# Kernel optimization log

Measured on AMD Instinct MI355X. Metric: run time of the kernel, lower is better.

Reference implementation:

```python
import jax, jax.numpy as jnp
import numpy as np

N = 100000
E = 1600000
IN_C = 128
HEADS = 4
HEAD_D = 32  # out_channels(128) // heads(4)


def setup_inputs() -> dict:
    key = jax.random.key(0)
    k1, k2, k3, k4, k5, k6 = jax.random.split(key, 6)
    x = jax.random.normal(k1, (N, IN_C), dtype=jnp.float32)
    edge_index = jax.random.randint(k2, (2, E), 0, N, dtype=jnp.int64)
    edge_weight = jax.random.uniform(k3, (E,), dtype=jnp.float32)
    # params: linear weight stored as [in, H*D] so forward is x @ W (torch does x @ weight.T)
    W = jax.random.normal(k4, (IN_C, HEADS * HEAD_D), dtype=jnp.float32) * (1.0 / np.sqrt(IN_C))
    att_src = jax.random.normal(k5, (HEADS, HEAD_D), dtype=jnp.float32) * 0.1
    att_dst = jax.random.normal(k6, (HEADS, HEAD_D), dtype=jnp.float32) * 0.1
    return {"x": x, "W": W, "att_src": att_src, "att_dst": att_dst,
            "edge_weight": edge_weight, "edge_index": edge_index, "num_nodes": N}


def reference(x, W, att_src, att_dst, edge_weight, edge_index, num_nodes):
    H, D = att_src.shape
    xw = (x @ W).reshape(-1, H, D)                       # [N, H, D]
    row, col = edge_index[0], edge_index[1]
    a_src = jnp.einsum('nhd,hd->nh', xw, att_src)        # [N, H]
    a_dst = jnp.einsum('nhd,hd->nh', xw, att_dst)        # [N, H]
    alpha = jax.nn.leaky_relu(a_src[row] + a_dst[col], negative_slope=0.2)  # [E, H]
    # segment softmax over edges grouped by row (destination of aggregation)
    amax = jax.ops.segment_max(alpha, row, num_segments=num_nodes)          # [N, H]
    amax = jnp.where(jnp.isfinite(amax), amax, 0.0)      # empty segments -> 0 (matches torch init)
    alpha = jnp.exp(alpha - amax[row])
    asum = jax.ops.segment_sum(alpha, row, num_segments=num_nodes)          # [N, H]
    alpha = alpha / (asum[row] + 1e-16)
    msg = xw[col] * alpha[..., None]                     # [E, H, D]
    out = jax.ops.segment_sum(msg, row, num_segments=num_nodes)             # [N, H, D]
    return out.reshape(num_nodes, H * D)
```

## Files before the change

### kernel.cpp

```cpp
#include <hip/hip_runtime.h>
#include <math.h>


typedef _Float16 half4 __attribute__((ext_vector_type(4)));
typedef _Float16 half8 __attribute__((ext_vector_type(8)));
typedef float    f32x4 __attribute__((ext_vector_type(4)));

#define PCHUNK   4096
#define NB_SHIFT 8
#define BCAP     4864

__device__ __forceinline__ float lrelu_exp(float v) {
    return __expf(fmaxf(v, 0.2f * v));
}

__global__ __launch_bounds__(256) void k_gemm(const float* __restrict__ x,
                                              const float* __restrict__ W,
                                              const float* __restrict__ att_src,
                                              const float* __restrict__ att_dst,
                                              _Float16* __restrict__ xwh,
                                              float* __restrict__ a_src,
                                              float* __restrict__ a_dst, int N) {
    __shared__ float Ws[32][128];
    __shared__ float xT[32][68];
    int t = threadIdx.x;
    int tx = t & 31;
    int ty = t >> 5;
    int row0 = blockIdx.x * 64;

    float acc[8][4];
    #pragma unroll
    for (int r = 0; r < 8; ++r)
        #pragma unroll
        for (int j = 0; j < 4; ++j) acc[r][j] = 0.f;

    for (int kc = 0; kc < 128; kc += 32) {
        __syncthreads();
        #pragma unroll
        for (int i = 0; i < 4; ++i) {
            int fi = i * 256 + t;
            int kl = fi >> 5, c4 = (fi & 31) << 2;
            *(float4*)&Ws[kl][c4] = *(const float4*)&W[(size_t)(kc + kl) * 128 + c4];
        }
        #pragma unroll
        for (int i = 0; i < 2; ++i) {
            int fi = i * 256 + t;
            int r = fi >> 3, kq = (fi & 7) << 2;
            int grow = row0 + r; if (grow >= N) grow = N - 1;
            float4 v = *(const float4*)&x[(size_t)grow * 128 + kc + kq];
            xT[kq + 0][r] = v.x;
            xT[kq + 1][r] = v.y;
            xT[kq + 2][r] = v.z;
            xT[kq + 3][r] = v.w;
        }
        __syncthreads();
        #pragma unroll 8
        for (int k = 0; k < 32; ++k) {
            float4 wv = *(const float4*)&Ws[k][tx << 2];
            float4 xa = *(const float4*)&xT[k][ty << 3];
            float4 xb = *(const float4*)&xT[k][(ty << 3) + 4];
            float xr[8] = {xa.x, xa.y, xa.z, xa.w, xb.x, xb.y, xb.z, xb.w};
            #pragma unroll
            for (int r = 0; r < 8; ++r) {
                acc[r][0] = fmaf(xr[r], wv.x, acc[r][0]);
                acc[r][1] = fmaf(xr[r], wv.y, acc[r][1]);
                acc[r][2] = fmaf(xr[r], wv.z, acc[r][2]);
                acc[r][3] = fmaf(xr[r], wv.w, acc[r][3]);
            }
        }
    }

    int h  = tx >> 3;
    int dq = (tx & 7) << 2;
    float4 as = *(const float4*)&att_src[h * 32 + dq];
    float4 ad = *(const float4*)&att_dst[h * 32 + dq];
    #pragma unroll
    for (int r = 0; r < 8; ++r) {
        int row = row0 + (ty << 3) + r;
        bool ok = row < N;
        if (ok) {
            half4 hv;
            hv.x = (_Float16)acc[r][0];
            hv.y = (_Float16)acc[r][1];
            hv.z = (_Float16)acc[r][2];
            hv.w = (_Float16)acc[r][3];
            *(half4*)&xwh[(size_t)row * 128 + (tx << 2)] = hv;
        }
        float ps = acc[r][0] * as.x + acc[r][1] * as.y + acc[r][2] * as.z + acc[r][3] * as.w;
        float pd = acc[r][0] * ad.x + acc[r][1] * ad.y + acc[r][2] * ad.z + acc[r][3] * ad.w;
        ps += __shfl_xor(ps, 1); pd += __shfl_xor(pd, 1);
        ps += __shfl_xor(ps, 2); pd += __shfl_xor(pd, 2);
        ps += __shfl_xor(ps, 4); pd += __shfl_xor(pd, 4);
        if (ok && (tx & 7) == 0) {
            a_src[(size_t)row * 4 + h] = ps;
            a_dst[(size_t)row * 4 + h] = pd;
        }
    }
}

__global__ __launch_bounds__(256) void k_part(const int* __restrict__ eidx,
                                              int* __restrict__ bctr,
                                              unsigned long long* __restrict__ rec,
                                              int E) {
    __shared__ unsigned long long buf[PCHUNK];
    __shared__ unsigned long long sbuf[PCHUNK];
    __shared__ int hist[512], excl[512], gbase[512], cur[512];
    __shared__ int wtot[4];
    int t = threadIdx.x;
    int lane = t & 63, wv = t >> 6;
    int e0 = blockIdx.x * PCHUNK;
    int nE = E - e0; if (nE > PCHUNK) nE = PCHUNK;
    hist[t] = 0; hist[t + 256] = 0;
    __syncthreads();
    for (int i = t; i < nE; i += 256) {
        int row = __builtin_nontemporal_load(&eidx[e0 + i]);
        int col = __builtin_nontemporal_load(&eidx[E + e0 + i]);
        buf[i] = ((unsigned long long)(unsigned)col << 32) | (unsigned)row;
        atomicAdd(&hist[row >> NB_SHIFT], 1);
    }
    __syncthreads();
    int h0 = hist[2 * t], h1 = hist[2 * t + 1];
    int s = h0 + h1, sc = s;
    #pragma unroll
    for (int off = 1; off < 64; off <<= 1) {
        int v = __shfl_up(sc, off);
        if (lane >= off) sc += v;
    }
    if (lane == 63) wtot[wv] = sc;
    __syncthreads();
    if (t == 0) {
        int run = 0;
        #pragma unroll
        for (int i = 0; i < 4; ++i) { int tmp = wtot[i]; wtot[i] = run; run += tmp; }
    }
    __syncthreads();
    int incl = sc + wtot[wv];
    excl[2 * t]     = incl - s;
    excl[2 * t + 1] = incl - h1;
    cur[2 * t]      = incl - s;
    cur[2 * t + 1]  = incl - h1;
    gbase[2 * t]     = h0 ? atomicAdd(&bctr[2 * t], h0) : 0;
    gbase[2 * t + 1] = h1 ? atomicAdd(&bctr[2 * t + 1], h1) : 0;
    __syncthreads();
    for (int i = t; i < nE; i += 256) {
        unsigned long long r = buf[i];
        int row = (int)(unsigned)r;
        int dst = atomicAdd(&cur[row >> NB_SHIFT], 1);
        sbuf[dst] = r;
    }
    __syncthreads();
    for (int j = t; j < nE; j += 256) {
        unsigned long long r = sbuf[j];
        int row = (int)(unsigned)r;
        int b = row >> NB_SHIFT;
        int off = gbase[b] + (j - excl[b]);
        if (off < BCAP)
            __builtin_nontemporal_store(r, &rec[(size_t)b * BCAP + off]);
    }
}

__global__ __launch_bounds__(256) void k_csr(const unsigned long long* __restrict__ rec,
                                             const int* __restrict__ bctr,
                                             int2* __restrict__ rseg,
                                             int* __restrict__ csr_col, int N) {
    __shared__ int cnt[256], cur[256];
    __shared__ int wtot[4];
    int b = blockIdx.x;
    int rs = b << NB_SHIFT;
    int t = threadIdx.x;
    int lane = t & 63, wv = t >> 6;
    cnt[t] = 0;
    __syncthreads();
    int m = bctr[b]; if (m > BCAP) m = BCAP;
    const unsigned long long* rr = &rec[(size_t)b * BCAP];
    for (int i = t; i < m; i += 256) {
        int row = (int)(unsigned)rr[i];
        atomicAdd(&cnt[row & 255], 1);
    }
    __syncthreads();
    int c = cnt[t], sc = c;
    #pragma unroll
    for (int off = 1; off < 64; off <<= 1) {
        int v = __shfl_up(sc, off);
        if (lane >= off) sc += v;
    }
    if (lane == 63) wtot[wv] = sc;
    __syncthreads();
    if (t == 0) {
        int run = 0;
        #pragma unroll
        for (int i = 0; i < 4; ++i) { int tmp = wtot[i]; wtot[i] = run; run += tmp; }
    }
    __syncthreads();
    int ex = sc + wtot[wv] - c;
    cur[t] = ex;
    int n = rs + t;
    if (n < N) {
        int2 sg;
        sg.x = b * BCAP + ex;
        sg.y = b * BCAP + ex + c;
        rseg[n] = sg;
    }
    __syncthreads();
    for (int i = t; i < m; i += 256) {
        unsigned long long r = rr[i];
        int row = (int)(unsigned)r;
        int col = (int)(r >> 32);
        int slot = atomicAdd(&cur[row & 255], 1);
        csr_col[b * BCAP + slot] = col;
    }
}

__global__ __launch_bounds__(256) void k_agg(const int2* __restrict__ rseg,
                                             const int* __restrict__ csr_col,
                                             const float* __restrict__ a_src,
                                             const float* __restrict__ a_dst,
                                             const _Float16* __restrict__ xwh,
                                             float* __restrict__ out, int N) {
    int lane = threadIdx.x & 63;
    int n = blockIdx.x * 4 + (threadIdx.x >> 6);
    if (n >= N) return;
    int2 seg = rseg[n];
    int beg = seg.x, end = seg.y;
    int q = lane >> 4;
    int l = lane & 15;
    int h = l >> 2;
    float s_n = a_src[(size_t)n * 4 + h];
    float acc[8] = {0, 0, 0, 0, 0, 0, 0, 0};
    float ws = 0.f;

    for (int w0 = beg; w0 < end; w0 += 64) {
        int rem = end - w0; if (rem > 64) rem = 64;
        int cc = (lane < rem) ? __builtin_nontemporal_load(&csr_col[w0 + lane]) : 0;
        int j = 0;
        for (; j + 16 <= rem; j += 16) {
            int c[4]; float ad[4]; half8 xv[4];
            #pragma unroll
            for (int u = 0; u < 4; ++u) c[u] = __shfl(cc, j + u * 4 + q);
            #pragma unroll
            for (int u = 0; u < 4; ++u) {
                ad[u] = a_dst[(size_t)c[u] * 4 + h];
                xv[u] = *(const half8*)&xwh[(size_t)c[u] * 128 + (l << 3)];
            }
            #pragma unroll
            for (int u = 0; u < 4; ++u) {
                float w = lrelu_exp(s_n + ad[u]);
                ws += w;
                #pragma unroll
                for (int k = 0; k < 8; ++k)
                    acc[k] += w * (float)xv[u][k];
            }
        }
        if (j < rem) {
            int c[4]; float m[4]; float ad[4]; half8 xv[4];
            #pragma unroll
            for (int u = 0; u < 4; ++u) {
                int r = j + u * 4 + q;
                c[u] = __shfl(cc, r);
                m[u] = (r < rem) ? 1.f : 0.f;
            }
            #pragma unroll
            for (int u = 0; u < 4; ++u) {
                ad[u] = a_dst[(size_t)c[u] * 4 + h];
                xv[u] = *(const half8*)&xwh[(size_t)c[u] * 128 + (l << 3)];
            }
            #pragma unroll
            for (int u = 0; u < 4; ++u) {
                float w = m[u] * lrelu_exp(s_n + ad[u]);
                ws += w;
                #pragma unroll
                for (int k = 0; k < 8; ++k)
                    acc[k] += w * (float)xv[u][k];
            }
        }
    }

    #pragma unroll
    for (int k = 0; k < 8; ++k) {
        acc[k] += __shfl_xor(acc[k], 16);
        acc[k] += __shfl_xor(acc[k], 32);
    }
    ws += __shfl_xor(ws, 16);
    ws += __shfl_xor(ws, 32);
    if (q == 0) {
        float inv = 1.0f / (ws + 1e-16f);
        f32x4 o0 = {acc[0] * inv, acc[1] * inv, acc[2] * inv, acc[3] * inv};
        f32x4 o1 = {acc[4] * inv, acc[5] * inv, acc[6] * inv, acc[7] * inv};
        __builtin_nontemporal_store(o0, (f32x4*)&out[(size_t)n * 128 + (l << 3)]);
        __builtin_nontemporal_store(o1, (f32x4*)&out[(size_t)n * 128 + (l << 3) + 4]);
    }
}

extern "C" void kernel_launch(void* const* d_in, const int* in_sizes, int n_in,
                              void* d_out, int out_size, void* d_ws, size_t ws_size,
                              hipStream_t stream) {
    const float* x       = (const float*)d_in[0];
    const float* W       = (const float*)d_in[1];
    const float* att_src = (const float*)d_in[2];
    const float* att_dst = (const float*)d_in[3];
    const int* eidx      = (const int*)d_in[5];
    int N = in_sizes[0] / 128;
    int E = in_sizes[4];
    float* out = (float*)d_out;

    char* p = (char*)d_ws;
    auto alloc = [&](size_t bytes) {
        char* r = p;
        p += (bytes + 255) & ~(size_t)255;
        return r;
    };
    int nbuckets = (N + 255) >> NB_SHIFT;
    _Float16* xwh  = (_Float16*)alloc((size_t)N * 128 * 2);
    float* a_src   = (float*)alloc((size_t)N * 4 * 4);
    float* a_dst   = (float*)alloc((size_t)N * 4 * 4);
    int*   bctr    = (int*)  alloc(512 * 4);
    unsigned long long* rec = (unsigned long long*)alloc((size_t)nbuckets * BCAP * 8);
    int2*  rseg    = (int2*) alloc((size_t)N * 8);
    int*   csr_col = (int*)  alloc((size_t)nbuckets * BCAP * 4);

    (void)hipMemsetAsync(bctr, 0, 512 * 4, stream);
    k_gemm<<<(N + 63) / 64, 256, 0, stream>>>(x, W, att_src, att_dst, xwh, a_src, a_dst, N);
    k_part<<<(E + PCHUNK - 1) / PCHUNK, 256, 0, stream>>>(eidx, bctr, rec, E);
    k_csr<<<nbuckets, 256, 0, stream>>>(rec, bctr, rseg, csr_col, N);
    k_agg<<<(N + 3) / 4, 256, 0, stream>>>(rseg, csr_col, a_src, a_dst, xwh, out, N);
}
```

Before: 271.1 us.

## Use MFMA fp16 GEMM for projection and process four nodes per wave in aggregation

The FP32 SIMT projection GEMM is replaced with an MFMA 16x16x32 fp16 kernel that converts x to half in swizzled LDS and reads a pre-transposed fp16 copy of W, prepared by a new small kernel. The aggregation kernel now gives each wave four consecutive destination nodes. When their combined edge lists fit in 128 entries it loads the column indices once and shares them by shuffle, and it sums four edges' contributions per step. This is meant to cut GEMM ALU time and per-node launch and index-load overhead, but rounding x and W to fp16 costs input precision.

```diff
diff --git a/kernel.cpp b/kernel.cpp
--- a/kernel.cpp
+++ b/kernel.cpp
@@ -14,86 +14,110 @@
     return __expf(fmaxf(v, 0.2f * v));
 }
 
+__global__ __launch_bounds__(128) void k_prep(const float* __restrict__ W,
+                                              _Float16* __restrict__ WTh) {
+    int n = blockIdx.x;
+    int k = threadIdx.x;
+    WTh[n * 128 + k] = (_Float16)W[(size_t)k * 128 + n];
+}
+
+__device__ __forceinline__ _Float16* lds_ptr(_Float16* base, int r, int kf16) {
+    int g = (kf16 >> 3) ^ (r & 7);
+    return base + r * 128 + g * 8 + (kf16 & 7);
+}
+
 __global__ __launch_bounds__(256) void k_gemm(const float* __restrict__ x,
-                                              const float* __restrict__ W,
+                                              const _Float16* __restrict__ WTh,
                                               const float* __restrict__ att_src,
                                               const float* __restrict__ att_dst,
                                               _Float16* __restrict__ xwh,
                                               float* __restrict__ a_src,
                                               float* __restrict__ a_dst, int N) {
-    __shared__ float Ws[32][128];
-    __shared__ float xT[32][68];
+    __shared__ _Float16 Xs[128 * 128];
+    __shared__ _Float16 Ws[128 * 128];
     int t = threadIdx.x;
-    int tx = t & 31;
-    int ty = t >> 5;
-    int row0 = blockIdx.x * 64;
-
-    float acc[8][4];
-    #pragma unroll
-    for (int r = 0; r < 8; ++r)
-        #pragma unroll
-        for (int j = 0; j < 4; ++j) acc[r][j] = 0.f;
-
-    for (int kc = 0; kc < 128; kc += 32) {
-        __syncthreads();
-        #pragma unroll
-        for (int i = 0; i < 4; ++i) {
-            int fi = i * 256 + t;
-            int kl = fi >> 5, c4 = (fi & 31) << 2;
-            *(float4*)&Ws[kl][c4] = *(const float4*)&W[(size_t)(kc + kl) * 128 + c4];
+    int lane = t & 63, wv = t >> 6;
+    int lm = lane & 15, lg = lane >> 4;
+    int row0 = blockIdx.x * 128;
+
+    #pragma unroll
+    for (int i = 0; i < 8; ++i) {
+        int f = (i * 256 + t) * 8;
+        int nr = f >> 7, kc = f & 127;
+        *(half8*)lds_ptr(Ws, nr, kc) = *(const half8*)&WTh[f];
+    }
+    #pragma unroll
+    for (int i = 0; i < 8; ++i) {
+        int f = (i * 256 + t) * 8;
+        int r = f >> 7, kc = f & 127;
+        int gr = row0 + r; if (gr >= N) gr = N - 1;
+        float4 v0 = *(const float4*)&x[(size_t)gr * 128 + kc];
+        float4 v1 = *(const float4*)&x[(size_t)gr * 128 + kc + 4];
+        half8 hv;
+        hv[0] = (_Float16)v0.x; hv[1] = (_Float16)v0.y;
+        hv[2] = (_Float16)v0.z; hv[3] = (_Float16)v0.w;
+        hv[4] = (_Float16)v1.x; hv[5] = (_Float16)v1.y;
+        hv[6] = (_Float16)v1.z; hv[7] = (_Float16)v1.w;
+        *(half8*)lds_ptr(Xs, r, kc) = hv;
+    }
+    __syncthreads();
+
+    f32x4 acc[2][8];
+    #pragma unroll
+    for (int m = 0; m < 2; ++m)
+        #pragma unroll
+        for (int nn = 0; nn < 8; ++nn) acc[m][nn] = (f32x4){0.f, 0.f, 0.f, 0.f};
+
+    #pragma unroll
+    for (int kk = 0; kk < 4; ++kk) {
+        int kb = kk * 32 + lg * 8;
+        half8 a0 = *(const half8*)lds_ptr(Xs, wv * 32 + lm, kb);
+        half8 a1 = *(const half8*)lds_ptr(Xs, wv * 32 + 16 + lm, kb);
+        half8 b[8];
+        #pragma unroll
+        for (int nn = 0; nn < 8; ++nn)
+            b[nn] = *(const half8*)lds_ptr(Ws, nn * 16 + lm, kb);
+        #pragma unroll
+        for (int nn = 0; nn < 8; ++nn) {
+            acc[0][nn] = __builtin_amdgcn_mfma_f32_16x16x32_f16(a0, b[nn], acc[0][nn], 0, 0, 0);
+            acc[1][nn] = __builtin_amdgcn_mfma_f32_16x16x32_f16(a1, b[nn], acc[1][nn], 0, 0, 0);
         }
-        #pragma unroll
-        for (int i = 0; i < 2; ++i) {
-            int fi = i * 256 + t;
-            int r = fi >> 3, kq = (fi & 7) << 2;
-            int grow = row0 + r; if (grow >= N) grow = N - 1;
-            float4 v = *(const float4*)&x[(size_t)grow * 128 + kc + kq];
-            xT[kq + 0][r] = v.x;
-            xT[kq + 1][r] = v.y;
-            xT[kq + 2][r] = v.z;
-            xT[kq + 3][r] = v.w;
-        }
-        __syncthreads();
-        #pragma unroll 8
-        for (int k = 0; k < 32; ++k) {
-            float4 wv = *(const float4*)&Ws[k][tx << 2];
-            float4 xa = *(const float4*)&xT[k][ty << 3];
-            float4 xb = *(const float4*)&xT[k][(ty << 3) + 4];
-            float xr[8] = {xa.x, xa.y, xa.z, xa.w, xb.x, xb.y, xb.z, xb.w};
+    }
+
+    float asv[8], adv[8];
+    #pragma unroll
+    for (int nn = 0; nn < 8; ++nn) {
+        asv[nn] = att_src[nn * 16 + lm];
+        adv[nn] = att_dst[nn * 16 + lm];
+    }
+    #pragma unroll
+    for (int m = 0; m < 2; ++m) {
+        #pragma unroll
+        for (int reg = 0; reg < 4; ++reg) {
+            int row = row0 + wv * 32 + m * 16 + lg * 4 + reg;
+            bool ok = row < N;
+            if (ok) {
+                #pragma unroll
+                for (int nn = 0; nn < 8; ++nn)
+                    xwh[(size_t)row * 128 + nn * 16 + lm] = (_Float16)acc[m][nn][reg];
+            }
+            float ps[4], pd[4];
             #pragma unroll
-            for (int r = 0; r < 8; ++r) {
-                acc[r][0] = fmaf(xr[r], wv.x, acc[r][0]);
-                acc[r][1] = fmaf(xr[r], wv.y, acc[r][1]);
-                acc[r][2] = fmaf(xr[r], wv.z, acc[r][2]);
-                acc[r][3] = fmaf(xr[r], wv.w, acc[r][3]);
-            }
-        }
-    }
-
-    int h  = tx >> 3;
-    int dq = (tx & 7) << 2;
-    float4 as = *(const float4*)&att_src[h * 32 + dq];
-    float4 ad = *(const float4*)&att_dst[h * 32 + dq];
-    #pragma unroll
-    for (int r = 0; r < 8; ++r) {
-        int row = row0 + (ty << 3) + r;
-        bool ok = row < N;
-        if (ok) {
-            half4 hv;
-            hv.x = (_Float16)acc[r][0];
-            hv.y = (_Float16)acc[r][1];
-            hv.z = (_Float16)acc[r][2];
-            hv.w = (_Float16)acc[r][3];
-            *(half4*)&xwh[(size_t)row * 128 + (tx << 2)] = hv;
-        }
-        float ps = acc[r][0] * as.x + acc[r][1] * as.y + acc[r][2] * as.z + acc[r][3] * as.w;
-        float pd = acc[r][0] * ad.x + acc[r][1] * ad.y + acc[r][2] * ad.z + acc[r][3] * ad.w;
-        ps += __shfl_xor(ps, 1); pd += __shfl_xor(pd, 1);
-        ps += __shfl_xor(ps, 2); pd += __shfl_xor(pd, 2);
-        ps += __shfl_xor(ps, 4); pd += __shfl_xor(pd, 4);
-        if (ok && (tx & 7) == 0) {
-            a_src[(size_t)row * 4 + h] = ps;
-            a_dst[(size_t)row * 4 + h] = pd;
+            for (int hh = 0; hh < 4; ++hh) {
+                ps[hh] = acc[m][2 * hh][reg] * asv[2 * hh] + acc[m][2 * hh + 1][reg] * asv[2 * hh + 1];
+                pd[hh] = acc[m][2 * hh][reg] * adv[2 * hh] + acc[m][2 * hh + 1][reg] * adv[2 * hh + 1];
+                #pragma unroll
+                for (int off = 1; off < 16; off <<= 1) {
+                    ps[hh] += __shfl_xor(ps[hh], off);
+                    pd[hh] += __shfl_xor(pd[hh], off);
+                }
+            }
+            if (ok && lm == 0) {
+                f32x4 vs = {ps[0], ps[1], ps[2], ps[3]};
+                f32x4 vd = {pd[0], pd[1], pd[2], pd[3]};
+                *(f32x4*)&a_src[(size_t)row * 4] = vs;
+                *(f32x4*)&a_dst[(size_t)row * 4] = vd;
+            }
         }
     }
 }
@@ -211,6 +235,32 @@
     }
 }
 
+#define EDGE4(C0, C1, C2, C3, M0, M1, M2, M3)                              \
+    {                                                                      \
+        float ad0 = a_dst[(size_t)(C0) * 4 + h];                           \
+        float ad1 = a_dst[(size_t)(C1) * 4 + h];                           \
+        float ad2 = a_dst[(size_t)(C2) * 4 + h];                           \
+        float ad3 = a_dst[(size_t)(C3) * 4 + h];                           \
+        half8 x0 = *(const half8*)&xwh[(size_t)(C0) * 128 + (l << 3)];     \
+        half8 x1 = *(const half8*)&xwh[(size_t)(C1) * 128 + (l << 3)];     \
+        half8 x2 = *(const half8*)&xwh[(size_t)(C2) * 128 + (l << 3)];     \
+        half8 x3 = *(const half8*)&xwh[(size_t)(C3) * 128 + (l << 3)];     \
+        float w0 = (M0) * lrelu_exp(s + ad0);                              \
+        float w1 = (M1) * lrelu_exp(s + ad1);                              \
+        float w2 = (M2) * lrelu_exp(s + ad2);                              \
+        float w3 = (M3) * lrelu_exp(s + ad3);                              \
+        ws += w0 + w1 + w2 + w3;                                           \
+        _Pragma("unroll")                                                  \
+        for (int kk = 0; kk < 8; ++kk)                                     \
+            acc[kk] += w0 * (float)x0[kk] + w1 * (float)x1[kk]             \
+                     + w2 * (float)x2[kk] + w3 * (float)x3[kk];            \
+    }
+
+#define FETCH2(IDX) ({ int _i = (IDX);                                     \
+                       int _c0 = __shfl(cc0, _i);                          \
+                       int _c1 = __shfl(cc1, _i - 64);                     \
+                       _i < 64 ? _c0 : _c1; })
+
 __global__ __launch_bounds__(256) void k_agg(const int2* __restrict__ rseg,
                                              const int* __restrict__ csr_col,
                                              const float* __restrict__ a_src,
@@ -218,76 +268,131 @@
                                              const _Float16* __restrict__ xwh,
                                              float* __restrict__ out, int N) {
     int lane = threadIdx.x & 63;
-    int n = blockIdx.x * 4 + (threadIdx.x >> 6);
-    if (n >= N) return;
-    int2 seg = rseg[n];
-    int beg = seg.x, end = seg.y;
+    int wv = threadIdx.x >> 6;
+    int n0 = (blockIdx.x * 4 + wv) * 4;
+    if (n0 >= N) return;
+    int nv = N - n0; if (nv > 4) nv = 4;
     int q = lane >> 4;
     int l = lane & 15;
     int h = l >> 2;
-    float s_n = a_src[(size_t)n * 4 + h];
-    float acc[8] = {0, 0, 0, 0, 0, 0, 0, 0};
-    float ws = 0.f;
-
-    for (int w0 = beg; w0 < end; w0 += 64) {
-        int rem = end - w0; if (rem > 64) rem = 64;
-        int cc = (lane < rem) ? __builtin_nontemporal_load(&csr_col[w0 + lane]) : 0;
-        int j = 0;
-        for (; j + 16 <= rem; j += 16) {
-            int c[4]; float ad[4]; half8 xv[4];
+
+    int begs[4], ends[4];
+    if (nv == 4) {
+        int4 sa = *(const int4*)&rseg[n0];
+        int4 sb = *(const int4*)&rseg[n0 + 2];
+        begs[0] = sa.x; ends[0] = sa.y; begs[1] = sa.z; ends[1] = sa.w;
+        begs[2] = sb.x; ends[2] = sb.y; begs[3] = sb.z; ends[3] = sb.w;
+    } else {
+        int2 s0 = rseg[n0];
+        begs[0] = s0.x; ends[0] = s0.y;
+        #pragma unroll
+        for (int j = 1; j < 4; ++j) {
+            if (j < nv) { int2 sj = rseg[n0 + j]; begs[j] = sj.x; ends[j] = sj.y; }
+            else        { begs[j] = ends[j - 1];  ends[j] = ends[j - 1]; }
+        }
+    }
+    float sn[4];
+    #pragma unroll
+    for (int j = 0; j < 4; ++j)
+        sn[j] = (j < nv) ? a_src[(size_t)(n0 + j) * 4 + h] : 0.f;
+
+    int base = begs[0];
+    int L = ends[3] - base;
+
+    if (L <= 128) {
+        int cc0 = (lane < L)      ? __builtin_nontemporal_load(&csr_col[base + lane])      : 0;
+        int cc1 = (lane + 64 < L) ? __builtin_nontemporal_load(&csr_col[base + 64 + lane]) : 0;
+        #pragma unroll
+        for (int j = 0; j < 4; ++j) {
+            float acc[8] = {0, 0, 0, 0, 0, 0, 0, 0};
+            float ws = 0.f;
+            float s = sn[j];
+            int deg = ends[j] - begs[j];
+            int o = begs[j] - base;
+            int i = 0;
+            for (; i + 16 <= deg; i += 16) {
+                int i0 = o + i + q;
+                int c0 = FETCH2(i0);
+                int c1 = FETCH2(i0 + 4);
+                int c2 = FETCH2(i0 + 8);
+                int c3 = FETCH2(i0 + 12);
+                EDGE4(c0, c1, c2, c3, 1.f, 1.f, 1.f, 1.f);
+            }
+            if (i < deg) {
+                int r0 = i + q, r1 = i + 4 + q, r2 = i + 8 + q, r3 = i + 12 + q;
+                float m0 = r0 < deg ? 1.f : 0.f;
+                float m1 = r1 < deg ? 1.f : 0.f;
+                float m2 = r2 < deg ? 1.f : 0.f;
+                float m3 = r3 < deg ? 1.f : 0.f;
+                int c0 = FETCH2(r0 < deg ? o + r0 : o);
+                int c1 = FETCH2(r1 < deg ? o + r1 : o);
+                int c2 = FETCH2(r2 < deg ? o + r2 : o);
+                int c3 = FETCH2(r3 < deg ? o + r3 : o);
+                EDGE4(c0, c1, c2, c3, m0, m1, m2, m3);
+            }
             #pragma unroll
-            for (int u = 0; u < 4; ++u) c[u] = __shfl(cc, j + u * 4 + q);
+            for (int kk = 0; kk < 8; ++kk) {
+                acc[kk] += __shfl_xor(acc[kk], 16);
+                acc[kk] += __shfl_xor(acc[kk], 32);
+            }
+            ws += __shfl_xor(ws, 16);
+            ws += __shfl_xor(ws, 32);
+            if (q == 0 && j < nv) {
+                int n = n0 + j;
+                float inv = 1.0f / (ws + 1e-16f);
+                f32x4 o0 = {acc[0] * inv, acc[1] * inv, acc[2] * inv, acc[3] * inv};
+                f32x4 o1 = {acc[4] * inv, acc[5] * inv, acc[6] * inv, acc[7] * inv};
+                __builtin_nontemporal_store(o0, (f32x4*)&out[(size_t)n * 128 + (l << 3)]);
+                __builtin_nontemporal_store(o1, (f32x4*)&out[(size_t)n * 128 + (l << 3) + 4]);
+            }
+        }
+    } else {
+        #pragma unroll
+        for (int j = 0; j < 4; ++j) {
+            float acc[8] = {0, 0, 0, 0, 0, 0, 0, 0};
+            float ws = 0.f;
+            float s = sn[j];
+            int beg = begs[j], end = ends[j];
+            for (int w0 = beg; w0 < end; w0 += 64) {
+                int rem = end - w0; if (rem > 64) rem = 64;
+                int cc = (lane < rem) ? __builtin_nontemporal_load(&csr_col[w0 + lane]) : 0;
+                int i = 0;
+                for (; i + 16 <= rem; i += 16) {
+                    int c0 = __shfl(cc, i + q);
+                    int c1 = __shfl(cc, i + 4 + q);
+                    int c2 = __shfl(cc, i + 8 + q);
+                    int c3 = __shfl(cc, i + 12 + q);
+                    EDGE4(c0, c1, c2, c3, 1.f, 1.f, 1.f, 1.f);
+                }
+                if (i < rem) {
+                    int r0 = i + q, r1 = i + 4 + q, r2 = i + 8 + q, r3 = i + 12 + q;
+                    float m0 = r0 < rem ? 1.f : 0.f;
+                    float m1 = r1 < rem ? 1.f : 0.f;
+                    float m2 = r2 < rem ? 1.f : 0.f;
+                    float m3 = r3 < rem ? 1.f : 0.f;
+                    int c0 = __shfl(cc, r0);
+                    int c1 = __shfl(cc, r1);
+                    int c2 = __shfl(cc, r2);
+                    int c3 = __shfl(cc, r3);
+                    EDGE4(c0, c1, c2, c3, m0, m1, m2, m3);
+                }
+            }
             #pragma unroll
-            for (int u = 0; u < 4; ++u) {
-                ad[u] = a_dst[(size_t)c[u] * 4 + h];
-                xv[u] = *(const half8*)&xwh[(size_t)c[u] * 128 + (l << 3)];
-            }
-            #pragma unroll
-            for (int u = 0; u < 4; ++u) {
-                float w = lrelu_exp(s_n + ad[u]);
-                ws += w;
-                #pragma unroll
-                for (int k = 0; k < 8; ++k)
-                    acc[k] += w * (float)xv[u][k];
+            for (int kk = 0; kk < 8; ++kk) {
+                acc[kk] += __shfl_xor(acc[kk], 16);
+                acc[kk] += __shfl_xor(acc[kk], 32);
+            }
+            ws += __shfl_xor(ws, 16);
+            ws += __shfl_xor(ws, 32);
+            if (q == 0 && j < nv) {
+                int n = n0 + j;
+                float inv = 1.0f / (ws + 1e-16f);
+                f32x4 o0 = {acc[0] * inv, acc[1] * inv, acc[2] * inv, acc[3] * inv};
+                f32x4 o1 = {acc[4] * inv, acc[5] * inv, acc[6] * inv, acc[7] * inv};
+                __builtin_nontemporal_store(o0, (f32x4*)&out[(size_t)n * 128 + (l << 3)]);
+                __builtin_nontemporal_store(o1, (f32x4*)&out[(size_t)n * 128 + (l << 3) + 4]);
             }
         }
-        if (j < rem) {
-            int c[4]; float m[4]; float ad[4]; half8 xv[4];
-            #pragma unroll
-            for (int u = 0; u < 4; ++u) {
-                int r = j + u * 4 + q;
-                c[u] = __shfl(cc, r);
-                m[u] = (r < rem) ? 1.f : 0.f;
-            }
-            #pragma unroll
-            for (int u = 0; u < 4; ++u) {
-                ad[u] = a_dst[(size_t)c[u] * 4 + h];
-                xv[u] = *(const half8*)&xwh[(size_t)c[u] * 128 + (l << 3)];
-            }
-            #pragma unroll
-            for (int u = 0; u < 4; ++u) {
-                float w = m[u] * lrelu_exp(s_n + ad[u]);
-                ws += w;
-                #pragma unroll
-                for (int k = 0; k < 8; ++k)
-                    acc[k] += w * (float)xv[u][k];
-            }
-        }
-    }
-
-    #pragma unroll
-    for (int k = 0; k < 8; ++k) {
-        acc[k] += __shfl_xor(acc[k], 16);
-        acc[k] += __shfl_xor(acc[k], 32);
-    }
-    ws += __shfl_xor(ws, 16);
-    ws += __shfl_xor(ws, 32);
-    if (q == 0) {
-        float inv = 1.0f / (ws + 1e-16f);
-        f32x4 o0 = {acc[0] * inv, acc[1] * inv, acc[2] * inv, acc[3] * inv};
-        f32x4 o1 = {acc[4] * inv, acc[5] * inv, acc[6] * inv, acc[7] * inv};
-        __builtin_nontemporal_store(o0, (f32x4*)&out[(size_t)n * 128 + (l << 3)]);
-        __builtin_nontemporal_store(o1, (f32x4*)&out[(size_t)n * 128 + (l << 3) + 4]);
     }
 }
 
@@ -317,10 +422,12 @@
     unsigned long long* rec = (unsigned long long*)alloc((size_t)nbuckets * BCAP * 8);
     int2*  rseg    = (int2*) alloc((size_t)N * 8);
     int*   csr_col = (int*)  alloc((size_t)nbuckets * BCAP * 4);
+    _Float16* WTh  = (_Float16*)alloc(128 * 128 * 2);
 
     (void)hipMemsetAsync(bctr, 0, 512 * 4, stream);
-    k_gemm<<<(N + 63) / 64, 256, 0, stream>>>(x, W, att_src, att_dst, xwh, a_src, a_dst, N);
+    k_prep<<<128, 128, 0, stream>>>(W, WTh);
+    k_gemm<<<(N + 127) / 128, 256, 0, stream>>>(x, WTh, att_src, att_dst, xwh, a_src, a_dst, N);
     k_part<<<(E + PCHUNK - 1) / PCHUNK, 256, 0, stream>>>(eidx, bctr, rec, E);
     k_csr<<<nbuckets, 256, 0, stream>>>(rec, bctr, rseg, csr_col, N);
-    k_agg<<<(N + 3) / 4, 256, 0, stream>>>(rseg, csr_col, a_src, a_dst, xwh, out, N);
-}
+    k_agg<<<(N + 15) / 16, 256, 0, stream>>>(rseg, csr_col, a_src, a_dst, xwh, out, N);
+}
```

Result: faster. 247.7 us (-8.6%).

## Use MFMA fp16 GEMM with folded attention columns and pack partition records

Applied to the files above, without the earlier changes.

The scalar fp32 GEMM is replaced by an MFMA 16x16x32 fp16 kernel. A small prep kernel transposes W to fp16 and appends W·att_src and W·att_dst columns, so the attention logits come out of the same matrix product. LDS is XOR-swizzled to avoid bank conflicts. Separately, partition records shrink from 64-bit (col,row) to 32-bit (col<<8 | row&255), which halves record traffic in k_part and k_csr; the bucket is recovered by binary search over the exclusive offsets. The fp16 inputs lower precision, and packing col<<8 assumes col < 2^24.

```diff
diff --git a/kernel.cpp b/kernel.cpp
--- a/kernel.cpp
+++ b/kernel.cpp
@@ -14,96 +14,103 @@
     return __expf(fmaxf(v, 0.2f * v));
 }
 
-__global__ __launch_bounds__(256) void k_gemm(const float* __restrict__ x,
-                                              const float* __restrict__ W,
+__global__ __launch_bounds__(128) void k_prep(const float* __restrict__ W,
                                               const float* __restrict__ att_src,
                                               const float* __restrict__ att_dst,
+                                              _Float16* __restrict__ Wa) {
+    int n = blockIdx.x;
+    int k = threadIdx.x;
+    float v;
+    if (n < 128) {
+        v = W[(size_t)k * 128 + n];
+    } else if (n < 136) {
+        int h = (n - 128) & 3;
+        const float* att = (n < 132) ? att_src : att_dst;
+        float s = 0.f;
+        #pragma unroll
+        for (int d = 0; d < 32; ++d)
+            s += W[(size_t)k * 128 + h * 32 + d] * att[h * 32 + d];
+        v = s;
+    } else {
+        v = 0.f;
+    }
+    Wa[n * 128 + k] = (_Float16)v;
+}
+
+__device__ __forceinline__ _Float16* lds_ptr(_Float16* base, int r, int kf16) {
+    int g = (kf16 >> 3) ^ (r & 7);
+    return base + r * 128 + g * 8 + (kf16 & 7);
+}
+
+__global__ __launch_bounds__(256) void k_gemm(const float* __restrict__ x,
+                                              const _Float16* __restrict__ Wa,
                                               _Float16* __restrict__ xwh,
                                               float* __restrict__ a_src,
                                               float* __restrict__ a_dst, int N) {
-    __shared__ float Ws[32][128];
-    __shared__ float xT[32][68];
+    __shared__ _Float16 Xs[64 * 128];
+    __shared__ _Float16 Ws[144 * 128];
     int t = threadIdx.x;
-    int tx = t & 31;
-    int ty = t >> 5;
+    int lane = t & 63, wv = t >> 6;
+    int lm = lane & 15, lg = lane >> 4;
     int row0 = blockIdx.x * 64;
 
-    float acc[8][4];
-    #pragma unroll
-    for (int r = 0; r < 8; ++r)
-        #pragma unroll
-        for (int j = 0; j < 4; ++j) acc[r][j] = 0.f;
-
-    for (int kc = 0; kc < 128; kc += 32) {
-        __syncthreads();
-        #pragma unroll
-        for (int i = 0; i < 4; ++i) {
-            int fi = i * 256 + t;
-            int kl = fi >> 5, c4 = (fi & 31) << 2;
-            *(float4*)&Ws[kl][c4] = *(const float4*)&W[(size_t)(kc + kl) * 128 + c4];
+    #pragma unroll
+    for (int i = 0; i < 9; ++i) {
+        int f = (i * 256 + t) * 8;
+        int nr = f >> 7, kc = f & 127;
+        *(half8*)lds_ptr(Ws, nr, kc) = *(const half8*)&Wa[f];
+    }
+    #pragma unroll
+    for (int i = 0; i < 4; ++i) {
+        int f = (i * 256 + t) * 8;
+        int r = f >> 7, kc = f & 127;
+        int gr = row0 + r; if (gr >= N) gr = N - 1;
+        float4 v0 = *(const float4*)&x[(size_t)gr * 128 + kc];
+        float4 v1 = *(const float4*)&x[(size_t)gr * 128 + kc + 4];
+        half8 hv;
+        hv[0] = (_Float16)v0.x; hv[1] = (_Float16)v0.y;
+        hv[2] = (_Float16)v0.z; hv[3] = (_Float16)v0.w;
+        hv[4] = (_Float16)v1.x; hv[5] = (_Float16)v1.y;
+        hv[6] = (_Float16)v1.z; hv[7] = (_Float16)v1.w;
+        *(half8*)lds_ptr(Xs, r, kc) = hv;
+    }
+    __syncthreads();
+
+    f32x4 acc[9];
+    #pragma unroll
+    for (int nn = 0; nn < 9; ++nn) acc[nn] = (f32x4){0.f, 0.f, 0.f, 0.f};
+
+    #pragma unroll
+    for (int kk = 0; kk < 4; ++kk) {
+        int kb = kk * 32 + lg * 8;
+        half8 a0 = *(const half8*)lds_ptr(Xs, wv * 16 + lm, kb);
+        #pragma unroll
+        for (int nn = 0; nn < 9; ++nn) {
+            half8 b = *(const half8*)lds_ptr(Ws, nn * 16 + lm, kb);
+            acc[nn] = __builtin_amdgcn_mfma_f32_16x16x32_f16(a0, b, acc[nn], 0, 0, 0);
         }
-        #pragma unroll
-        for (int i = 0; i < 2; ++i) {
-            int fi = i * 256 + t;
-            int r = fi >> 3, kq = (fi & 7) << 2;
-            int grow = row0 + r; if (grow >= N) grow = N - 1;
-            float4 v = *(const float4*)&x[(size_t)grow * 128 + kc + kq];
-            xT[kq + 0][r] = v.x;
-            xT[kq + 1][r] = v.y;
-            xT[kq + 2][r] = v.z;
-            xT[kq + 3][r] = v.w;
-        }
-        __syncthreads();
-        #pragma unroll 8
-        for (int k = 0; k < 32; ++k) {
-            float4 wv = *(const float4*)&Ws[k][tx << 2];
-            float4 xa = *(const float4*)&xT[k][ty << 3];
-            float4 xb = *(const float4*)&xT[k][(ty << 3) + 4];
-            float xr[8] = {xa.x, xa.y, xa.z, xa.w, xb.x, xb.y, xb.z, xb.w};
-            #pragma unroll
-            for (int r = 0; r < 8; ++r) {
-                acc[r][0] = fmaf(xr[r], wv.x, acc[r][0]);
-                acc[r][1] = fmaf(xr[r], wv.y, acc[r][1]);
-                acc[r][2] = fmaf(xr[r], wv.z, acc[r][2]);
-                acc[r][3] = fmaf(xr[r], wv.w, acc[r][3]);
-            }
-        }
-    }
-
-    int h  = tx >> 3;
-    int dq = (tx & 7) << 2;
-    float4 as = *(const float4*)&att_src[h * 32 + dq];
-    float4 ad = *(const float4*)&att_dst[h * 32 + dq];
-    #pragma unroll
-    for (int r = 0; r < 8; ++r) {
-        int row = row0 + (ty << 3) + r;
-        bool ok = row < N;
-        if (ok) {
-            half4 hv;
-            hv.x = (_Float16)acc[r][0];
-            hv.y = (_Float16)acc[r][1];
-            hv.z = (_Float16)acc[r][2];
-            hv.w = (_Float16)acc[r][3];
-            *(half4*)&xwh[(size_t)row * 128 + (tx << 2)] = hv;
-        }
-        float ps = acc[r][0] * as.x + acc[r][1] * as.y + acc[r][2] * as.z + acc[r][3] * as.w;
-        float pd = acc[r][0] * ad.x + acc[r][1] * ad.y + acc[r][2] * ad.z + acc[r][3] * ad.w;
-        ps += __shfl_xor(ps, 1); pd += __shfl_xor(pd, 1);
-        ps += __shfl_xor(ps, 2); pd += __shfl_xor(pd, 2);
-        ps += __shfl_xor(ps, 4); pd += __shfl_xor(pd, 4);
-        if (ok && (tx & 7) == 0) {
-            a_src[(size_t)row * 4 + h] = ps;
-            a_dst[(size_t)row * 4 + h] = pd;
+    }
+
+    #pragma unroll
+    for (int reg = 0; reg < 4; ++reg) {
+        int row = row0 + wv * 16 + lg * 4 + reg;
+        if (row < N) {
+            #pragma unroll
+            for (int nn = 0; nn < 8; ++nn)
+                xwh[(size_t)row * 128 + nn * 16 + lm] = (_Float16)acc[nn][reg];
+            float lv = acc[8][reg];
+            if (lm < 4)      a_src[(size_t)row * 4 + lm]       = lv;
+            else if (lm < 8) a_dst[(size_t)row * 4 + (lm - 4)] = lv;
         }
     }
 }
 
 __global__ __launch_bounds__(256) void k_part(const int* __restrict__ eidx,
                                               int* __restrict__ bctr,
-                                              unsigned long long* __restrict__ rec,
+                                              unsigned* __restrict__ rec,
                                               int E) {
     __shared__ unsigned long long buf[PCHUNK];
-    __shared__ unsigned long long sbuf[PCHUNK];
+    __shared__ unsigned sbuf[PCHUNK];
     __shared__ int hist[512], excl[512], gbase[512], cur[512];
     __shared__ int wtot[4];
     int t = threadIdx.x;
@@ -146,20 +153,23 @@
         unsigned long long r = buf[i];
         int row = (int)(unsigned)r;
         int dst = atomicAdd(&cur[row >> NB_SHIFT], 1);
-        sbuf[dst] = r;
+        sbuf[dst] = ((unsigned)(r >> 32) << 8) | ((unsigned)row & 255u);
     }
     __syncthreads();
     for (int j = t; j < nE; j += 256) {
-        unsigned long long r = sbuf[j];
-        int row = (int)(unsigned)r;
-        int b = row >> NB_SHIFT;
+        unsigned r = sbuf[j];
+        int lo = 0;
+        #pragma unroll
+        for (int stp = 256; stp >= 1; stp >>= 1)
+            if (lo + stp <= 511 && excl[lo + stp] <= j) lo += stp;
+        int b = lo;
         int off = gbase[b] + (j - excl[b]);
         if (off < BCAP)
             __builtin_nontemporal_store(r, &rec[(size_t)b * BCAP + off]);
     }
 }
 
-__global__ __launch_bounds__(256) void k_csr(const unsigned long long* __restrict__ rec,
+__global__ __launch_bounds__(256) void k_csr(const unsigned* __restrict__ rec,
                                              const int* __restrict__ bctr,
                                              int2* __restrict__ rseg,
                                              int* __restrict__ csr_col, int N) {
@@ -172,10 +182,10 @@
     cnt[t] = 0;
     __syncthreads();
     int m = bctr[b]; if (m > BCAP) m = BCAP;
-    const unsigned long long* rr = &rec[(size_t)b * BCAP];
+    const unsigned* rr = &rec[(size_t)b * BCAP];
     for (int i = t; i < m; i += 256) {
-        int row = (int)(unsigned)rr[i];
-        atomicAdd(&cnt[row & 255], 1);
+        unsigned r = rr[i];
+        atomicAdd(&cnt[r & 255u], 1);
     }
     __syncthreads();
     int c = cnt[t], sc = c;
@@ -203,11 +213,9 @@
     }
     __syncthreads();
     for (int i = t; i < m; i += 256) {
-        unsigned long long r = rr[i];
-        int row = (int)(unsigned)r;
-        int col = (int)(r >> 32);
-        int slot = atomicAdd(&cur[row & 255], 1);
-        csr_col[b * BCAP + slot] = col;
+        unsigned r = rr[i];
+        int slot = atomicAdd(&cur[r & 255u], 1);
+        csr_col[b * BCAP + slot] = (int)(r >> 8);
     }
 }
 
@@ -314,12 +322,14 @@
     float* a_src   = (float*)alloc((size_t)N * 4 * 4);
     float* a_dst   = (float*)alloc((size_t)N * 4 * 4);
     int*   bctr    = (int*)  alloc(512 * 4);
-    unsigned long long* rec = (unsigned long long*)alloc((size_t)nbuckets * BCAP * 8);
+    unsigned* rec  = (unsigned*)alloc((size_t)nbuckets * BCAP * 4);
     int2*  rseg    = (int2*) alloc((size_t)N * 8);
     int*   csr_col = (int*)  alloc((size_t)nbuckets * BCAP * 4);
+    _Float16* Wa   = (_Float16*)alloc(144 * 128 * 2);
 
     (void)hipMemsetAsync(bctr, 0, 512 * 4, stream);
-    k_gemm<<<(N + 63) / 64, 256, 0, stream>>>(x, W, att_src, att_dst, xwh, a_src, a_dst, N);
+    k_prep<<<144, 128, 0, stream>>>(W, att_src, att_dst, Wa);
+    k_gemm<<<(N + 63) / 64, 256, 0, stream>>>(x, Wa, xwh, a_src, a_dst, N);
     k_part<<<(E + PCHUNK - 1) / PCHUNK, 256, 0, stream>>>(eidx, bctr, rec, E);
     k_csr<<<nbuckets, 256, 0, stream>>>(rec, bctr, rseg, csr_col, N);
     k_agg<<<(N + 3) / 4, 256, 0, stream>>>(rseg, csr_col, a_src, a_dst, xwh, out, N);
```

After: 240.7 us. -11.2%, faster.
